# Optimization experiments

Hardware: AMD Instinct MI355X
Metric: run time of the kernel (lower is better)

Reference implementation:

```python
import jax, jax.numpy as jnp
import numpy as np

N = 50000      # nodes
E = 800000     # edges (avg degree 16)
IN, H, C = 256, 128, 64
LPA_ITER = 10


def setup_inputs() -> dict:
    key = jax.random.key(0)
    ks = jax.random.split(key, 8)
    x = jax.random.normal(ks[0], (N, IN), dtype=jnp.float32)
    soft_labels = jax.random.uniform(ks[1], (N, C), dtype=jnp.float32)
    edge_index = jax.random.randint(ks[2], (2, E), 0, N, dtype=jnp.int64)
    edge_attr = jax.random.uniform(ks[3], (E,), dtype=jnp.float32)  # abs(edge_weights), positive
    W1 = jax.random.normal(ks[4], (IN, H), dtype=jnp.float32) * (1.0 / np.sqrt(IN))
    b1 = jnp.zeros((H,), dtype=jnp.float32)
    W2 = jax.random.normal(ks[5], (H, C), dtype=jnp.float32) * (1.0 / np.sqrt(H))
    b2 = jnp.zeros((C,), dtype=jnp.float32)
    return {"x": x, "soft_labels": soft_labels, "edge_index": edge_index,
            "edge_attr": edge_attr, "W1": W1, "b1": b1, "W2": W2, "b2": b2}


def reference(x, soft_labels, edge_index, edge_attr, W1, b1, W2, b2):
    row, col = edge_index[0], edge_index[1]
    # Row-normalize sparse adjacency: deg[i] = sum of edge values in row i,
    # value <- value / deg[row]  (deg^-1 with inf -> 0)
    deg = jax.ops.segment_sum(edge_attr, row, num_segments=N)
    deg_inv = jnp.where(deg > 0, 1.0 / deg, 0.0)
    val = edge_attr * deg_inv[row]  # [E]

    def spmm(m):
        # out[i] = sum_{(i,j) in E} A[i,j] * m[j]
        return jax.ops.segment_sum(val[:, None] * m[col], row, num_segments=N)

    # GCNConv(normalize=False): spmm(A, x @ W) + b ; dropout is identity in eval mode
    h = jax.nn.relu(spmm(x @ W1) + b1)
    out = spmm(h @ W2) + b2

    # Label propagation: lpa_iter sparse-dense spmm steps
    labels = soft_labels
    for _ in range(LPA_ITER):
        labels = spmm(labels)
    return out, labels
```

## Files before the change

kernel.cpp:

```cpp
#include <hip/hip_runtime.h>

#define NN 50000
#define EE 800000
#define FIN 256
#define FH 128
#define FC 64
#define LPA_ITERS 10
#define NBLK 196
#define G1X 782
#define SPB 3125
#define SP128B 6250

typedef __attribute__((ext_vector_type(8))) short short8v;
typedef __attribute__((ext_vector_type(4))) float f32x4;

__device__ __forceinline__ int edge_at(const int* __restrict__ ei, int is32, int which, int e) {
    int idx = which * EE + e;
    return is32 ? ei[idx] : ei[2 * idx];
}

__global__ void detect_k(const unsigned int* __restrict__ w, int* __restrict__ flag) {
    int any = 0;
    for (int i = 1 + 2 * (int)threadIdx.x; i < 2048; i += 2 * (int)blockDim.x)
        if (w[i] != 0u) any = 1;
    if (any) atomicOr(flag, 1);
}

__device__ __forceinline__ unsigned short bf16_rne(float f) {
    unsigned u = __float_as_uint(f);
    return (unsigned short)((u + 0x7FFFu + ((u >> 16) & 1u)) >> 16);
}
__device__ __forceinline__ unsigned packbf2(float a, float b) {
    return (unsigned)bf16_rne(a) | ((unsigned)bf16_rne(b) << 16);
}

__global__ __launch_bounds__(256) void accum_k(const int* __restrict__ ei,
                                               const int* __restrict__ flag,
                                               int* __restrict__ cnt,
                                               int* __restrict__ slot) {
    int e = blockIdx.x * 256 + threadIdx.x;
    if (e >= EE) return;
    int is32 = *flag;
    int r = edge_at(ei, is32, 0, e);
    slot[e] = atomicAdd(&cnt[r], 1);
}

__global__ __launch_bounds__(256) void scan1_k(const int* __restrict__ cnt,
                                               int* __restrict__ start,
                                               int* __restrict__ bsum,
                                               int* __restrict__ blockhist) {
    __shared__ int wtot[4];
    __shared__ int hist[64];
    int t = threadIdx.x, blk = blockIdx.x;
    int i = blk * 256 + t;
    if (t < 64) hist[t] = 0;
    __syncthreads();
    int c = (i < NN) ? cnt[i] : 0;
    if (i < NN) atomicAdd(&hist[c < 63 ? c : 63], 1);
    int lane = t & 63, w = t >> 6;
    int s = c;
    for (int d = 1; d < 64; d <<= 1) {
        int u = __shfl_up(s, d, 64);
        if (lane >= d) s += u;
    }
    if (lane == 63) wtot[w] = s;
    __syncthreads();
    int woff = 0;
    for (int j = 0; j < 4; ++j)
        if (j < w) woff += wtot[j];
    int excl = s - c + woff;
    if (i < NN) start[i] = excl;
    if (t == 255) bsum[blk] = excl + c;
    if (t < 64) blockhist[t * NBLK + blk] = hist[t];
}

__global__ void scan2_k(int* __restrict__ bsum, int* __restrict__ blockhist) {
    __shared__ int wtot[4];
    __shared__ int btot[64];
    int t = threadIdx.x;
    int lane = t & 63, w = t >> 6;
    int v = (t < NBLK) ? bsum[t] : 0;
    int s = v;
    for (int d = 1; d < 64; d <<= 1) {
        int u = __shfl_up(s, d, 64);
        if (lane >= d) s += u;
    }
    if (lane == 63) wtot[w] = s;
    __syncthreads();
    int woff = 0;
    for (int j = 0; j < 4; ++j)
        if (j < w) woff += wtot[j];
    if (t < NBLK) bsum[t] = s - v + woff;
    if (t < 64) {
        int run = 0;
        for (int j = 0; j < NBLK; ++j) {
            int idx = t * NBLK + j;
            int tmp = blockhist[idx];
            blockhist[idx] = run;
            run += tmp;
        }
        btot[t] = run;
    }
    __syncthreads();
    if (t < 64) {
        int bv = btot[t];
        int bs = bv;
        for (int d = 1; d < 64; d <<= 1) {
            int u = __shfl_up(bs, d, 64);
            if (lane >= d) bs += u;
        }
        int base = bs - bv;
        for (int j = 0; j < NBLK; ++j) blockhist[t * NBLK + j] += base;
    }
}

__global__ __launch_bounds__(256) void finish_k(const int* __restrict__ cnt,
                                                int* __restrict__ start,
                                                const int* __restrict__ bsum,
                                                const int* __restrict__ blockhist,
                                                int* __restrict__ perm) {
    __shared__ int hist[64];
    int t = threadIdx.x, blk = blockIdx.x;
    int i = blk * 256 + t;
    if (t < 64) hist[t] = 0;
    __syncthreads();
    if (i < NN) {
        start[i] += bsum[blk];
        int c = cnt[i];
        int b = c < 63 ? c : 63;
        int rank = atomicAdd(&hist[b], 1);
        perm[blockhist[b * NBLK + blk] + rank] = i;
    }
}

__global__ __launch_bounds__(256) void scatter_k(const int* __restrict__ ei,
                                                 const int* __restrict__ flag,
                                                 const float* __restrict__ ea,
                                                 const int* __restrict__ start,
                                                 const int* __restrict__ slot,
                                                 uint2* __restrict__ csr) {
    int e = blockIdx.x * 256 + threadIdx.x;
    if (e >= EE) return;
    int is32 = *flag;
    int r = edge_at(ei, is32, 0, e);
    int c = edge_at(ei, is32, 1, e);
    csr[start[r] + slot[e]] = make_uint2((unsigned)c, __float_as_uint(ea[e]));
}

__global__ __launch_bounds__(256) void rowscale_k(const int* __restrict__ start,
                                                  const int* __restrict__ cnt,
                                                  const uint2* __restrict__ csr,
                                                  float* __restrict__ deginv) {
    int t = threadIdx.x;
    int r = blockIdx.x * 16 + (t >> 4);
    if (r >= NN) return;
    int fl = t & 15;
    int s = start[r], n = cnt[r];
    float sum = 0.f;
    for (int k = fl; k < n; k += 16) sum += __uint_as_float(csr[s + k].y);
    for (int d = 1; d < 16; d <<= 1) sum += __shfl_xor(sum, d, 16);
    if (fl == 0) deginv[r] = sum > 0.f ? 1.f / sum : 0.f;
}

__global__ __launch_bounds__(256) void wcvt_k(const float* __restrict__ W,
                                              short* __restrict__ hi,
                                              short* __restrict__ lo,
                                              int K, int N) {
    int i = blockIdx.x * 256 + threadIdx.x;
    if (i >= K * N) return;
    int k = i / N, n = i - k * N;
    float f = W[i];
    unsigned short h = bf16_rne(f);
    float hf = __uint_as_float((unsigned)h << 16);
    unsigned short l = bf16_rne(f - hf);
    hi[n * K + k] = (short)h;
    lo[n * K + k] = (short)l;
}

__global__ __launch_bounds__(256) void cast_k(const float* __restrict__ in,
                                              uint2* __restrict__ outb, int n4) {
    int i = blockIdx.x * 256 + threadIdx.x;
    if (i >= n4) return;
    float4 f = ((const float4*)in)[i];
    outb[i] = make_uint2(packbf2(f.x, f.y), packbf2(f.z, f.w));
}


template <int KDIM, int NCOLT, int NF, int ABF, int CBF>
__device__ __forceinline__ void mgemm2_body(int bx, int cb,
                                            const void* __restrict__ Ap,
                                            const short* __restrict__ Bhi0,
                                            const short* __restrict__ Blo0,
                                            void* __restrict__ Cp, int M) {
    static_assert((size_t)NF * 16 * 72 * 2 * 2 < 49152, "LDS must stay well under 64KB");
    __shared__ short bh[NF * 16][72];
    __shared__ short bl[NF * 16][72];
    const int NSTG = KDIM / 64;
    const int NCH = NF / 2;
    int t = threadIdx.x;
    const short* Bhi = Bhi0 + (size_t)cb * (NF * 16) * KDIM;
    const short* Blo = Blo0 + (size_t)cb * (NF * 16) * KDIM;
    int wid = t >> 6, l = t & 63, l15 = l & 15, lq = l >> 4;
    int row = bx * 64 + wid * 16 + l15;
    bool rv = row < M;
    f32x4 acc[NF];
#pragma unroll
    for (int j = 0; j < NF; ++j) acc[j] = (f32x4){0.f, 0.f, 0.f, 0.f};

    short8v rh[NCH], rl[NCH];
    float4 af[2][4];
    short8v ab_[2][2];
#pragma unroll
    for (int b = 0; b < 2; ++b) {
        if (ABF) {
            ab_[b][0] = (short8v){0, 0, 0, 0, 0, 0, 0, 0};
            ab_[b][1] = (short8v){0, 0, 0, 0, 0, 0, 0, 0};
        } else {
#pragma unroll
            for (int q = 0; q < 4; ++q) af[b][q] = make_float4(0.f, 0.f, 0.f, 0.f);
        }
    }

    auto loadB = [&](int k0) {
#pragma unroll
        for (int j = 0; j < NCH; ++j) {
            int c = t + j * 256;
            int col = c >> 3;
            int kk = (c & 7) * 8;
            rh[j] = *(const short8v*)&Bhi[(size_t)col * KDIM + k0 + kk];
            rl[j] = *(const short8v*)&Blo[(size_t)col * KDIM + k0 + kk];
        }
    };
    auto loadA = [&](int k0, int buf) {
        if (!rv) return;
        if (ABF) {
            const short* A = (const short*)Ap;
            ab_[buf][0] = *(const short8v*)&A[(size_t)row * KDIM + k0 + 8 * lq];
            ab_[buf][1] = *(const short8v*)&A[(size_t)row * KDIM + k0 + 32 + 8 * lq];
        } else {
            const float* A = (const float*)Ap;
            const float4* p0 = (const float4*)&A[(size_t)row * KDIM + k0 + 8 * lq];
            af[buf][0] = p0[0];
            af[buf][1] = p0[1];
            const float4* p1 = (const float4*)&A[(size_t)row * KDIM + k0 + 32 + 8 * lq];
            af[buf][2] = p1[0];
            af[buf][3] = p1[1];
        }
    };

    loadB(0);
    loadA(0, 0);
#pragma unroll
    for (int sg = 0; sg < NSTG; ++sg) {
        __syncthreads();
#pragma unroll
        for (int j = 0; j < NCH; ++j) {
            int c = t + j * 256;
            int col = c >> 3;
            int kk = (c & 7) * 8;
            *(short8v*)&bh[col][kk] = rh[j];
            *(short8v*)&bl[col][kk] = rl[j];
        }
        __syncthreads();
        if (sg + 1 < NSTG) {
            loadB((sg + 1) * 64);
            loadA((sg + 1) * 64, (sg + 1) & 1);
        }
        int cbuf = sg & 1;
#pragma unroll
        for (int ks = 0; ks < 2; ++ks) {
            short8v ahi, alo;
            if (ABF) {
                ahi = ab_[cbuf][ks];
            } else {
                float av[8];
                float4 xa = af[cbuf][ks * 2], xb = af[cbuf][ks * 2 + 1];
                av[0] = xa.x; av[1] = xa.y; av[2] = xa.z; av[3] = xa.w;
                av[4] = xb.x; av[5] = xb.y; av[6] = xb.z; av[7] = xb.w;
#pragma unroll
                for (int e = 0; e < 8; ++e) {
                    unsigned short h = bf16_rne(av[e]);
                    float hf = __uint_as_float((unsigned)h << 16);
                    ahi[e] = (short)h;
                    alo[e] = (short)bf16_rne(av[e] - hf);
                }
            }
#pragma unroll
            for (int j = 0; j < NF; ++j) {
                int col = j * 16 + l15;
                short8v fh = *(const short8v*)&bh[col][ks * 32 + 8 * lq];
                short8v fo = *(const short8v*)&bl[col][ks * 32 + 8 * lq];
                acc[j] = __builtin_amdgcn_mfma_f32_16x16x32_bf16(ahi, fh, acc[j], 0, 0, 0);
                acc[j] = __builtin_amdgcn_mfma_f32_16x16x32_bf16(ahi, fo, acc[j], 0, 0, 0);
                if (!ABF)
                    acc[j] = __builtin_amdgcn_mfma_f32_16x16x32_bf16(alo, fh, acc[j], 0, 0, 0);
            }
        }
    }
    int rbase = bx * 64 + wid * 16 + 4 * lq;
#pragma unroll
    for (int j = 0; j < NF; ++j) {
        int col = cb * (NF * 16) + j * 16 + l15;
#pragma unroll
        for (int e = 0; e < 4; ++e) {
            int r = rbase + e;
            if (r < M) {
                if (CBF)
                    ((unsigned short*)Cp)[(size_t)r * NCOLT + col] = bf16_rne(acc[j][e]);
                else
                    ((float*)Cp)[(size_t)r * NCOLT + col] = acc[j][e];
            }
        }
    }
}

__device__ __forceinline__ void spmm64f_body(int pb, const int* __restrict__ perm,
                                             const int* __restrict__ start,
                                             const int* __restrict__ cnt,
                                             const float* __restrict__ deginv,
                                             const uint2* __restrict__ csr,
                                             const float* __restrict__ m,
                                             float* __restrict__ out,
                                             const float* __restrict__ bias) {
    int t = threadIdx.x;
    int p = pb * 16 + (t >> 4);
    if (p >= NN) return;
    int r = perm[p];
    int fl = t & 15;
    const float4* m4 = (const float4*)m;
    float4 acc = make_float4(0.f, 0.f, 0.f, 0.f);
    int s = start[r], n = cnt[r];
    int k = 0;
    for (; k + 8 <= n; k += 8) {
        uint2 ev[8];
        float4 gv[8];
#pragma unroll
        for (int u = 0; u < 8; ++u) ev[u] = csr[s + k + u];
#pragma unroll
        for (int u = 0; u < 8; ++u) gv[u] = m4[(size_t)ev[u].x * 16 + fl];
#pragma unroll
        for (int u = 0; u < 8; ++u) {
            float v = __uint_as_float(ev[u].y);
            acc.x = fmaf(v, gv[u].x, acc.x); acc.y = fmaf(v, gv[u].y, acc.y);
            acc.z = fmaf(v, gv[u].z, acc.z); acc.w = fmaf(v, gv[u].w, acc.w);
        }
    }
    for (; k < n; ++k) {
        uint2 e = csr[s + k];
        float v = __uint_as_float(e.y);
        float4 g = m4[(size_t)e.x * 16 + fl];
        acc.x = fmaf(v, g.x, acc.x); acc.y = fmaf(v, g.y, acc.y);
        acc.z = fmaf(v, g.z, acc.z); acc.w = fmaf(v, g.w, acc.w);
    }
    float dv = deginv[r];
    acc.x *= dv; acc.y *= dv; acc.z *= dv; acc.w *= dv;
    float4 b = ((const float4*)bias)[fl];
    acc.x += b.x; acc.y += b.y; acc.z += b.z; acc.w += b.w;
    ((float4*)out)[(size_t)r * 16 + fl] = acc;
}

__device__ __forceinline__ void spmm128b_body(int pb, const int* __restrict__ perm,
                                              const int* __restrict__ start,
                                              const int* __restrict__ cnt,
                                              const float* __restrict__ deginv,
                                              const uint2* __restrict__ csr,
                                              const uint2* __restrict__ mb,
                                              uint2* __restrict__ outb,
                                              const float* __restrict__ bias) {
    int t = threadIdx.x;
    int p = pb * 8 + (t >> 5);
    if (p >= NN) return;
    int r = perm[p];
    int fl = t & 31;
    float4 acc = make_float4(0.f, 0.f, 0.f, 0.f);
    int s = start[r], n = cnt[r];
    int k = 0;
    for (; k + 8 <= n; k += 8) {
        uint2 ev[8];
        uint2 gv[8];
#pragma unroll
        for (int u = 0; u < 8; ++u) ev[u] = csr[s + k + u];
#pragma unroll
        for (int u = 0; u < 8; ++u) gv[u] = mb[(size_t)ev[u].x * 32 + fl];
#pragma unroll
        for (int u = 0; u < 8; ++u) {
            float v = __uint_as_float(ev[u].y);
            acc.x = fmaf(v, __uint_as_float(gv[u].x << 16), acc.x);
            acc.y = fmaf(v, __uint_as_float(gv[u].x & 0xFFFF0000u), acc.y);
            acc.z = fmaf(v, __uint_as_float(gv[u].y << 16), acc.z);
            acc.w = fmaf(v, __uint_as_float(gv[u].y & 0xFFFF0000u), acc.w);
        }
    }
    for (; k < n; ++k) {
        uint2 e = csr[s + k];
        float v = __uint_as_float(e.y);
        uint2 g = mb[(size_t)e.x * 32 + fl];
        acc.x = fmaf(v, __uint_as_float(g.x << 16), acc.x);
        acc.y = fmaf(v, __uint_as_float(g.x & 0xFFFF0000u), acc.y);
        acc.z = fmaf(v, __uint_as_float(g.y << 16), acc.z);
        acc.w = fmaf(v, __uint_as_float(g.y & 0xFFFF0000u), acc.w);
    }
    float dv = deginv[r];
    float4 b = ((const float4*)bias)[fl];
    acc.x = fmaxf(fmaf(acc.x, dv, b.x), 0.f);
    acc.y = fmaxf(fmaf(acc.y, dv, b.y), 0.f);
    acc.z = fmaxf(fmaf(acc.z, dv, b.z), 0.f);
    acc.w = fmaxf(fmaf(acc.w, dv, b.w), 0.f);
    outb[(size_t)r * 32 + fl] = make_uint2(packbf2(acc.x, acc.y), packbf2(acc.z, acc.w));
}

__device__ __forceinline__ void spmm64b_body(int pb, const int* __restrict__ perm,
                                             const int* __restrict__ start,
                                             const int* __restrict__ cnt,
                                             const float* __restrict__ deginv,
                                             const uint2* __restrict__ csr,
                                             const uint2* __restrict__ mb,
                                             void* __restrict__ outp, int f32out) {
    int t = threadIdx.x;
    int p = pb * 16 + (t >> 4);
    if (p >= NN) return;
    int r = perm[p];
    int fl = t & 15;
    float4 acc = make_float4(0.f, 0.f, 0.f, 0.f);
    int s = start[r], n = cnt[r];
    int k = 0;
    for (; k + 8 <= n; k += 8) {
        uint2 ev[8];
        uint2 gv[8];
#pragma unroll
        for (int u = 0; u < 8; ++u) ev[u] = csr[s + k + u];
#pragma unroll
        for (int u = 0; u < 8; ++u) gv[u] = mb[(size_t)ev[u].x * 16 + fl];
#pragma unroll
        for (int u = 0; u < 8; ++u) {
            float v = __uint_as_float(ev[u].y);
            acc.x = fmaf(v, __uint_as_float(gv[u].x << 16), acc.x);
            acc.y = fmaf(v, __uint_as_float(gv[u].x & 0xFFFF0000u), acc.y);
            acc.z = fmaf(v, __uint_as_float(gv[u].y << 16), acc.z);
            acc.w = fmaf(v, __uint_as_float(gv[u].y & 0xFFFF0000u), acc.w);
        }
    }
    for (; k < n; ++k) {
        uint2 e = csr[s + k];
        float v = __uint_as_float(e.y);
        uint2 g = mb[(size_t)e.x * 16 + fl];
        acc.x = fmaf(v, __uint_as_float(g.x << 16), acc.x);
        acc.y = fmaf(v, __uint_as_float(g.x & 0xFFFF0000u), acc.y);
        acc.z = fmaf(v, __uint_as_float(g.y << 16), acc.z);
        acc.w = fmaf(v, __uint_as_float(g.y & 0xFFFF0000u), acc.w);
    }
    float dv = deginv[r];
    acc.x *= dv; acc.y *= dv; acc.z *= dv; acc.w *= dv;
    if (f32out) {
        ((float4*)outp)[(size_t)r * 16 + fl] = acc;
    } else {
        ((uint2*)outp)[(size_t)r * 16 + fl] =
            make_uint2(packbf2(acc.x, acc.y), packbf2(acc.z, acc.w));
    }
}


__global__ __launch_bounds__(256) void f1_k(const float* __restrict__ x,
                                            const short* __restrict__ w1h,
                                            const short* __restrict__ w1l,
                                            unsigned short* __restrict__ t1,
                                            const int* __restrict__ perm,
                                            const int* __restrict__ start,
                                            const int* __restrict__ cnt,
                                            const float* __restrict__ dinv,
                                            const uint2* __restrict__ csr,
                                            const uint2* __restrict__ sbf,
                                            uint2* __restrict__ lA) {
    int b = blockIdx.x;
    if (b < 2 * G1X)
        mgemm2_body<FIN, FH, 4, 0, 1>(b % G1X, b / G1X, x, w1h, w1l, t1, NN);
    else
        spmm64b_body(b - 2 * G1X, perm, start, cnt, dinv, csr, sbf, lA, 0);
}

__global__ __launch_bounds__(256) void f2_k(const int* __restrict__ perm,
                                            const int* __restrict__ start,
                                            const int* __restrict__ cnt,
                                            const float* __restrict__ dinv,
                                            const uint2* __restrict__ csr,
                                            const uint2* __restrict__ t1,
                                            uint2* __restrict__ h,
                                            const float* __restrict__ b1,
                                            const uint2* __restrict__ lA,
                                            uint2* __restrict__ lB) {
    int b = blockIdx.x;
    if (b < SP128B)
        spmm128b_body(b, perm, start, cnt, dinv, csr, t1, h, b1);
    else
        spmm64b_body(b - SP128B, perm, start, cnt, dinv, csr, lA, lB, 0);
}

__global__ __launch_bounds__(256) void f3_k(const unsigned short* __restrict__ h,
                                            const short* __restrict__ w2h,
                                            const short* __restrict__ w2l,
                                            float* __restrict__ t2,
                                            const int* __restrict__ perm,
                                            const int* __restrict__ start,
                                            const int* __restrict__ cnt,
                                            const float* __restrict__ dinv,
                                            const uint2* __restrict__ csr,
                                            const uint2* __restrict__ lB,
                                            uint2* __restrict__ lA) {
    int b = blockIdx.x;
    if (b < G1X)
        mgemm2_body<FH, FC, 4, 1, 0>(b, 0, h, w2h, w2l, t2, NN);
    else
        spmm64b_body(b - G1X, perm, start, cnt, dinv, csr, lB, lA, 0);
}

__global__ __launch_bounds__(256) void f4_k(const int* __restrict__ perm,
                                            const int* __restrict__ start,
                                            const int* __restrict__ cnt,
                                            const float* __restrict__ dinv,
                                            const uint2* __restrict__ csr,
                                            const float* __restrict__ t2,
                                            float* __restrict__ out,
                                            const float* __restrict__ b2,
                                            const uint2* __restrict__ lA,
                                            uint2* __restrict__ lB) {
    int b = blockIdx.x;
    if (b < SPB)
        spmm64f_body(b, perm, start, cnt, dinv, csr, t2, out, b2);
    else
        spmm64b_body(b - SPB, perm, start, cnt, dinv, csr, lA, lB, 0);
}

__global__ __launch_bounds__(256) void spmm64b_k(const int* __restrict__ perm,
                                                 const int* __restrict__ start,
                                                 const int* __restrict__ cnt,
                                                 const float* __restrict__ deginv,
                                                 const uint2* __restrict__ csr,
                                                 const uint2* __restrict__ mb,
                                                 void* __restrict__ outp,
                                                 int f32out) {
    spmm64b_body(blockIdx.x, perm, start, cnt, deginv, csr, mb, outp, f32out);
}

extern "C" void kernel_launch(void* const* d_in, const int* in_sizes, int n_in,
                              void* d_out, int out_size, void* d_ws, size_t ws_size,
                              hipStream_t stream) {
    const float* x    = (const float*)d_in[0];
    const float* soft = (const float*)d_in[1];
    const int*   ei   = (const int*)d_in[2];
    const float* ea   = (const float*)d_in[3];
    const float* W1   = (const float*)d_in[4];
    const float* b1   = (const float*)d_in[5];
    const float* W2   = (const float*)d_in[6];
    const float* b2   = (const float*)d_in[7];
    float* out  = (float*)d_out;
    float* labB = out + (size_t)NN * FC;

    char* ws = (char*)d_ws;
    size_t off = 0;
    auto alloc = [&](size_t b) { size_t o = off; off += (b + 255) & ~(size_t)255; return o; };
    size_t o_misc  = alloc(256);
    size_t o_cnt   = alloc((size_t)NN * 4);
    size_t zero_end = off;
    size_t o_start = alloc((size_t)NN * 4);
    size_t o_perm  = alloc((size_t)NN * 4);
    size_t o_dinv  = alloc((size_t)NN * 4);
    size_t o_bsum  = alloc((size_t)NBLK * 4);
    size_t o_bhist = alloc((size_t)64 * NBLK * 4);
    size_t o_slot  = alloc((size_t)EE * 4);
    size_t o_csr   = alloc((size_t)EE * 8);
    size_t o_w1h   = alloc((size_t)FIN * FH * 2);
    size_t o_w1l   = alloc((size_t)FIN * FH * 2);
    size_t o_w2h   = alloc((size_t)FH * FC * 2);
    size_t o_w2l   = alloc((size_t)FH * FC * 2);
    size_t o_t1    = alloc((size_t)NN * FH * 2);
    size_t o_h     = alloc((size_t)NN * FH * 2);
    size_t o_t2    = alloc((size_t)NN * FC * 4);
    size_t o_sbf   = alloc((size_t)NN * FC * 2);
    size_t o_lA    = alloc((size_t)NN * FC * 2);
    size_t o_lB    = alloc((size_t)NN * FC * 2);
    if (off > ws_size) return;

    int*   misc  = (int*)(ws + o_misc);
    int*   cnt   = (int*)(ws + o_cnt);
    int*   start = (int*)(ws + o_start);
    int*   perm  = (int*)(ws + o_perm);
    float* dinv  = (float*)(ws + o_dinv);
    int*   bsum  = (int*)(ws + o_bsum);
    int*   bhist = (int*)(ws + o_bhist);
    int*   slot  = (int*)(ws + o_slot);
    uint2* csr   = (uint2*)(ws + o_csr);
    short* w1h   = (short*)(ws + o_w1h);
    short* w1l   = (short*)(ws + o_w1l);
    short* w2h   = (short*)(ws + o_w2h);
    short* w2l   = (short*)(ws + o_w2l);
    unsigned short* t1 = (unsigned short*)(ws + o_t1);
    uint2* h     = (uint2*)(ws + o_h);
    float* t2    = (float*)(ws + o_t2);
    uint2* sbf   = (uint2*)(ws + o_sbf);
    uint2* lA    = (uint2*)(ws + o_lA);
    uint2* lB    = (uint2*)(ws + o_lB);

    hipMemsetAsync(d_ws, 0, zero_end, stream);
    detect_k<<<1, 256, 0, stream>>>((const unsigned int*)ei, &misc[0]);
    accum_k<<<(EE + 255) / 256, 256, 0, stream>>>(ei, misc, cnt, slot);
    scan1_k<<<NBLK, 256, 0, stream>>>(cnt, start, bsum, bhist);
    scan2_k<<<1, 256, 0, stream>>>(bsum, bhist);
    finish_k<<<NBLK, 256, 0, stream>>>(cnt, start, bsum, bhist, perm);
    scatter_k<<<(EE + 255) / 256, 256, 0, stream>>>(ei, misc, ea, start, slot, csr);
    rowscale_k<<<(NN + 15) / 16, 256, 0, stream>>>(start, cnt, csr, dinv);
    wcvt_k<<<(FIN * FH + 255) / 256, 256, 0, stream>>>(W1, w1h, w1l, FIN, FH);
    wcvt_k<<<(FH * FC + 255) / 256, 256, 0, stream>>>(W2, w2h, w2l, FH, FC);
    cast_k<<<(NN * FC / 4 + 255) / 256, 256, 0, stream>>>(soft, sbf, NN * FC / 4);

    f1_k<<<2 * G1X + SPB, 256, 0, stream>>>(x, w1h, w1l, t1, perm, start, cnt, dinv,
                                            csr, sbf, lA);
    f2_k<<<SP128B + SPB, 256, 0, stream>>>(perm, start, cnt, dinv, csr,
                                           (const uint2*)t1, h, b1, lA, lB);
    f3_k<<<G1X + SPB, 256, 0, stream>>>((const unsigned short*)h, w2h, w2l, t2,
                                        perm, start, cnt, dinv, csr, lB, lA);
    f4_k<<<SPB + SPB, 256, 0, stream>>>(perm, start, cnt, dinv, csr, t2, out, b2,
                                        lA, lB);

    const uint2* src = lB;
    uint2* dst = lA;
    for (int it = 4; it < LPA_ITERS; ++it) {
        int last = (it == LPA_ITERS - 1);
        spmm64b_k<<<SPB, 256, 0, stream>>>(perm, start, cnt, dinv, csr, src,
                                           last ? (void*)labB : (void*)dst, last);
        src = dst;
        dst = (dst == lA) ? lB : lA;
    }
}
```

Measured before the change: 358.9 us.

## Overlap edge-count accumulation with first GEMM, shift LPA overlap later

The first GEMM (x@W1) no longer depends on the CSR build, so it now runs in the same fused launch as the edge-count atomic accumulation, ahead of the scan and scatter steps. The first label-propagation step moves into f2, which means only three LPA steps overlap with the GCN kernels and seven run standalone instead of six. This hides the GEMM behind the CSR construction at the cost of one extra standalone SpMM launch and a reordered buffer ping-pong.

New measurement: 350.9 us. -2.2%, faster.

```diff
diff --git a/kernel.cpp b/kernel.cpp
--- a/kernel.cpp
+++ b/kernel.cpp
@@ -10,6 +10,7 @@
 #define G1X 782
 #define SPB 3125
 #define SP128B 6250
+#define EBLK 3125
 
 typedef __attribute__((ext_vector_type(8))) short short8v;
 typedef __attribute__((ext_vector_type(4))) float f32x4;
@@ -34,11 +35,11 @@
     return (unsigned)bf16_rne(a) | ((unsigned)bf16_rne(b) << 16);
 }
 
-__global__ __launch_bounds__(256) void accum_k(const int* __restrict__ ei,
-                                               const int* __restrict__ flag,
-                                               int* __restrict__ cnt,
-                                               int* __restrict__ slot) {
-    int e = blockIdx.x * 256 + threadIdx.x;
+__device__ __forceinline__ void accum_body(int pb, const int* __restrict__ ei,
+                                           const int* __restrict__ flag,
+                                           int* __restrict__ cnt,
+                                           int* __restrict__ slot) {
+    int e = pb * 256 + (int)threadIdx.x;
     if (e >= EE) return;
     int is32 = *flag;
     int r = edge_at(ei, is32, 0, e);
@@ -460,22 +461,19 @@
 }
 
 
-__global__ __launch_bounds__(256) void f1_k(const float* __restrict__ x,
+__global__ __launch_bounds__(256) void fa_k(const float* __restrict__ x,
                                             const short* __restrict__ w1h,
                                             const short* __restrict__ w1l,
                                             unsigned short* __restrict__ t1,
-                                            const int* __restrict__ perm,
-                                            const int* __restrict__ start,
-                                            const int* __restrict__ cnt,
-                                            const float* __restrict__ dinv,
-                                            const uint2* __restrict__ csr,
-                                            const uint2* __restrict__ sbf,
-                                            uint2* __restrict__ lA) {
+                                            const int* __restrict__ ei,
+                                            const int* __restrict__ flag,
+                                            int* __restrict__ cnt,
+                                            int* __restrict__ slot) {
     int b = blockIdx.x;
     if (b < 2 * G1X)
         mgemm2_body<FIN, FH, 4, 0, 1>(b % G1X, b / G1X, x, w1h, w1l, t1, NN);
     else
-        spmm64b_body(b - 2 * G1X, perm, start, cnt, dinv, csr, sbf, lA, 0);
+        accum_body(b - 2 * G1X, ei, flag, cnt, slot);
 }
 
 __global__ __launch_bounds__(256) void f2_k(const int* __restrict__ perm,
@@ -486,13 +484,13 @@
                                             const uint2* __restrict__ t1,
                                             uint2* __restrict__ h,
                                             const float* __restrict__ b1,
-                                            const uint2* __restrict__ lA,
-                                            uint2* __restrict__ lB) {
+                                            const uint2* __restrict__ sbf,
+                                            uint2* __restrict__ lA) {
     int b = blockIdx.x;
     if (b < SP128B)
         spmm128b_body(b, perm, start, cnt, dinv, csr, t1, h, b1);
     else
-        spmm64b_body(b - SP128B, perm, start, cnt, dinv, csr, lA, lB, 0);
+        spmm64b_body(b - SP128B, perm, start, cnt, dinv, csr, sbf, lA, 0);
 }
 
 __global__ __launch_bounds__(256) void f3_k(const unsigned short* __restrict__ h,
@@ -504,13 +502,13 @@
                                             const int* __restrict__ cnt,
                                             const float* __restrict__ dinv,
                                             const uint2* __restrict__ csr,
-                                            const uint2* __restrict__ lB,
-                                            uint2* __restrict__ lA) {
+                                            const uint2* __restrict__ lA,
+                                            uint2* __restrict__ lB) {
     int b = blockIdx.x;
     if (b < G1X)
         mgemm2_body<FH, FC, 4, 1, 0>(b, 0, h, w2h, w2l, t2, NN);
     else
-        spmm64b_body(b - G1X, perm, start, cnt, dinv, csr, lB, lA, 0);
+        spmm64b_body(b - G1X, perm, start, cnt, dinv, csr, lA, lB, 0);
 }
 
 __global__ __launch_bounds__(256) void f4_k(const int* __restrict__ perm,
@@ -521,13 +519,13 @@
                                             const float* __restrict__ t2,
                                             float* __restrict__ out,
                                             const float* __restrict__ b2,
-                                            const uint2* __restrict__ lA,
-                                            uint2* __restrict__ lB) {
+                                            const uint2* __restrict__ lB,
+                                            uint2* __restrict__ lA) {
     int b = blockIdx.x;
     if (b < SPB)
         spmm64f_body(b, perm, start, cnt, dinv, csr, t2, out, b2);
     else
-        spmm64b_body(b - SPB, perm, start, cnt, dinv, csr, lA, lB, 0);
+        spmm64b_body(b - SPB, perm, start, cnt, dinv, csr, lB, lA, 0);
 }
 
 __global__ __launch_bounds__(256) void spmm64b_k(const int* __restrict__ perm,
@@ -602,28 +600,28 @@
 
     hipMemsetAsync(d_ws, 0, zero_end, stream);
     detect_k<<<1, 256, 0, stream>>>((const unsigned int*)ei, &misc[0]);
-    accum_k<<<(EE + 255) / 256, 256, 0, stream>>>(ei, misc, cnt, slot);
+    wcvt_k<<<(FIN * FH + 255) / 256, 256, 0, stream>>>(W1, w1h, w1l, FIN, FH);
+    wcvt_k<<<(FH * FC + 255) / 256, 256, 0, stream>>>(W2, w2h, w2l, FH, FC);
+    cast_k<<<(NN * FC / 4 + 255) / 256, 256, 0, stream>>>(soft, sbf, NN * FC / 4);
+
+    fa_k<<<2 * G1X + EBLK, 256, 0, stream>>>(x, w1h, w1l, t1, ei, misc, cnt, slot);
+
     scan1_k<<<NBLK, 256, 0, stream>>>(cnt, start, bsum, bhist);
     scan2_k<<<1, 256, 0, stream>>>(bsum, bhist);
     finish_k<<<NBLK, 256, 0, stream>>>(cnt, start, bsum, bhist, perm);
     scatter_k<<<(EE + 255) / 256, 256, 0, stream>>>(ei, misc, ea, start, slot, csr);
     rowscale_k<<<(NN + 15) / 16, 256, 0, stream>>>(start, cnt, csr, dinv);
-    wcvt_k<<<(FIN * FH + 255) / 256, 256, 0, stream>>>(W1, w1h, w1l, FIN, FH);
-    wcvt_k<<<(FH * FC + 255) / 256, 256, 0, stream>>>(W2, w2h, w2l, FH, FC);
-    cast_k<<<(NN * FC / 4 + 255) / 256, 256, 0, stream>>>(soft, sbf, NN * FC / 4);
-
-    f1_k<<<2 * G1X + SPB, 256, 0, stream>>>(x, w1h, w1l, t1, perm, start, cnt, dinv,
-                                            csr, sbf, lA);
+
     f2_k<<<SP128B + SPB, 256, 0, stream>>>(perm, start, cnt, dinv, csr,
-                                           (const uint2*)t1, h, b1, lA, lB);
+                                           (const uint2*)t1, h, b1, sbf, lA);
     f3_k<<<G1X + SPB, 256, 0, stream>>>((const unsigned short*)h, w2h, w2l, t2,
-                                        perm, start, cnt, dinv, csr, lB, lA);
+                                        perm, start, cnt, dinv, csr, lA, lB);
     f4_k<<<SPB + SPB, 256, 0, stream>>>(perm, start, cnt, dinv, csr, t2, out, b2,
-                                        lA, lB);
-
-    const uint2* src = lB;
-    uint2* dst = lA;
-    for (int it = 4; it < LPA_ITERS; ++it) {
+                                        lB, lA);
+
+    const uint2* src = lA;
+    uint2* dst = lB;
+    for (int it = 3; it < LPA_ITERS; ++it) {
         int last = (it == LPA_ITERS - 1);
         spmm64b_k<<<SPB, 256, 0, stream>>>(perm, start, cnt, dinv, csr, src,
                                            last ? (void*)labB : (void*)dst, last);
```
